# Kernel optimization log

Measured on AMD Instinct MI355X. Metric: run time of the kernel, lower is better.

Reference implementation:

```python
import jax, jax.numpy as jnp
import numpy as np

N_P, N_HE, N_E = 50000, 5000, 800000
D_IN, D_HID, D_OUT = 128, 256, 128
N_HEADS = 4
HEAD_DIM = D_HID // N_HEADS  # 64


def setup_inputs() -> dict:
    key = jax.random.key(0)
    ks = jax.random.split(key, 20)

    def xav(k, shape):
        fan_in, fan_out = shape[-2], shape[-1]
        lim = (6.0 / (fan_in + fan_out)) ** 0.5
        return jax.random.uniform(k, shape, jnp.float32, -lim, lim)

    return {
        "feat": jax.random.normal(ks[0], (N_P, D_IN), jnp.float32),
        "edge_w": jax.random.uniform(ks[1], (N_E,), jnp.float32),
        "Wself": xav(ks[2], (D_IN, D_OUT)), "bself": jnp.zeros((D_OUT,), jnp.float32),
        "Wclu": xav(ks[3], (D_IN, D_OUT)), "bclu": jnp.zeros((D_OUT,), jnp.float32),
        # 4 attention heads, each: Linear(D_IN->HEAD_DIM) -> ReLU -> Linear(HEAD_DIM->1) -> Sigmoid
        "Wh1": xav(ks[4], (N_HEADS, D_IN, HEAD_DIM)), "bh1": jnp.zeros((N_HEADS, HEAD_DIM), jnp.float32),
        "Wh2": xav(ks[5], (N_HEADS, HEAD_DIM, 1))[..., 0], "bh2": jnp.zeros((N_HEADS,), jnp.float32),
        "Wfuse": xav(ks[6], (N_HEADS, 1)),  # attn_fusion, no bias
        # fusion_attention MLP: 2*D_OUT -> D_HID -> D_HID//2 -> 2, softmax
        "Wf1": xav(ks[7], (2 * D_OUT, D_HID)), "bf1": jnp.zeros((D_HID,), jnp.float32),
        "Wf2": xav(ks[8], (D_HID, D_HID // 2)), "bf2": jnp.zeros((D_HID // 2,), jnp.float32),
        "Wf3": xav(ks[9], (D_HID // 2, 2)), "bf3": jnp.zeros((2,), jnp.float32),
        "edge_pid": jax.random.randint(ks[10], (N_E,), 0, N_P, jnp.int32),
        "edge_hid": jax.random.randint(ks[11], (N_E,), 0, N_HE, jnp.int32),
        "n_hyperedges": N_HE,
    }


def reference(feat, edge_w, Wself, bself, Wclu, bclu, Wh1, bh1, Wh2, bh2,
              Wfuse, Wf1, bf1, Wf2, bf2, Wf3, bf3,
              edge_pid, edge_hid, n_hyperedges):
    n_proteins = feat.shape[0]
    ew = edge_w[:, None]
    # Pass 1: protein -> hyperedge weighted gather-scatter (u_mul_e + sum)
    he_feat = jax.ops.segment_sum(feat[edge_pid] * ew, edge_hid, num_segments=n_hyperedges)  # [n_he, D_IN]
    # Multi-head MLP attention over hyperedge features
    h = jax.nn.relu(jnp.einsum('nd,hdk->hnk', he_feat, Wh1) + bh1[:, None, :])  # [H, n_he, hd]
    attn = jax.nn.sigmoid(jnp.einsum('hnk,hk->hn', h, Wh2) + bh2[:, None])      # [H, n_he]
    he_attn = attn.T @ Wfuse                                                    # [n_he, 1]
    he_weighted = he_feat * he_attn
    # Pass 2: hyperedge -> protein weighted gather-scatter
    cluster_feat = jax.ops.segment_sum(he_weighted[edge_hid] * ew, edge_pid, num_segments=n_proteins)  # [N, D_IN]
    # Transforms + fusion attention
    self_f = feat @ Wself + bself
    clu_f = cluster_feat @ Wclu + bclu
    cat = jnp.concatenate([self_f, clu_f], axis=-1)
    fw = jax.nn.softmax(
        jax.nn.relu(jax.nn.relu(cat @ Wf1 + bf1) @ Wf2 + bf2) @ Wf3 + bf3, axis=-1)  # [N, 2]
    fused = self_f * fw[:, 0:1] + clu_f * fw[:, 1:2]
    # residual: input_dim == output_dim so residual_proj is None (identity)
    return jax.nn.relu(fused + feat)
```

## Files before the change

### kernel.cpp

```cpp
#include <hip/hip_runtime.h>

#define N_P 50000
#define N_HE 5000
#define N_E 800000
#define D_IN 128
#define D_HID 256
#define N_HEADS 4
#define HEAD_DIM 64
#define CAP_HE 320
#define CAP_P  64
#define NTILE_TOT 3125
#define NCHUNK 782
#define CS2 264

typedef __attribute__((ext_vector_type(8))) short short8;
typedef __attribute__((ext_vector_type(8))) _Float16 half8;
typedef __attribute__((ext_vector_type(4))) float f32x4;

__device__ __forceinline__ short f2bs(float x) {
    union { float f; unsigned u; } v; v.f = x;
    unsigned r = (v.u + 0x7FFFu + ((v.u >> 16) & 1u)) >> 16;
    return (short)r;
}
__device__ __forceinline__ float bs2f(short s) {
    union { unsigned u; float f; } v; v.u = ((unsigned)(unsigned short)s) << 16;
    return v.f;
}
__device__ __forceinline__ short f2hs(float x) {
    union { _Float16 h; short s; } v; v.h = (_Float16)x; return v.s;
}

__global__ void k_zero_int(int* __restrict__ p, unsigned n) {
    unsigned i = blockIdx.x * blockDim.x + threadIdx.x;
    unsigned stride = gridDim.x * blockDim.x;
    for (; i < n; i += stride) p[i] = 0;
}

__global__ void k_prep(
    const float* __restrict__ Wself, const float* __restrict__ Wclu,
    const float* __restrict__ Wf1,   const float* __restrict__ Wf2,
    short* __restrict__ WselfT_hi, short* __restrict__ WselfT_lo,
    short* __restrict__ WcluT_hi,  short* __restrict__ WcluT_lo,
    short* __restrict__ Wf1T_h,
    short* __restrict__ Wf2T_h) {
    unsigned i = blockIdx.x * 256u + threadIdx.x;
    if (i < 16384u) {
        unsigned j = i >> 7, d = i & 127u;
        float v = Wself[d * 128 + j];
        short h = f2bs(v);
        WselfT_hi[i] = h; WselfT_lo[i] = f2bs(v - bs2f(h));
    } else if (i < 32768u) {
        unsigned ii = i - 16384u, j = ii >> 7, d = ii & 127u;
        float v = Wclu[d * 128 + j];
        short h = f2bs(v);
        WcluT_hi[ii] = h; WcluT_lo[ii] = f2bs(v - bs2f(h));
    } else if (i < 98304u) {
        unsigned ii = i - 32768u, j = ii >> 8, d = ii & 255u;
        Wf1T_h[ii] = f2hs(Wf1[d * 256 + j]);
    } else {
        unsigned ii = i - 98304u, j = ii >> 8, d = ii & 255u;
        Wf2T_h[ii] = f2hs(Wf2[d * 128 + j]);
    }
}

__global__ void k_bucket(
    const int* __restrict__ edge_pid, const int* __restrict__ edge_hid,
    const float* __restrict__ edge_w,
    int* __restrict__ cnt_he, int* __restrict__ cnt_p,
    int2* __restrict__ list_he, int2* __restrict__ list_p,
    int* __restrict__ ovf_he, int* __restrict__ ovf_he_cnt,
    int* __restrict__ ovf_p,  int* __restrict__ ovf_p_cnt) {
    unsigned e = blockIdx.x * blockDim.x + threadIdx.x;
    unsigned stride = gridDim.x * blockDim.x;
    for (; e < N_E; e += stride) {
        int h = edge_hid[e], p = edge_pid[e];
        int wbits = __float_as_int(edge_w[e]);
        int pos = atomicAdd(cnt_he + h, 1);
        if (pos < CAP_HE) list_he[h * CAP_HE + pos] = make_int2(p, wbits);
        else              ovf_he[atomicAdd(ovf_he_cnt, 1)] = (int)e;
        int pp = atomicAdd(cnt_p + p, 1);
        if (pp < CAP_P)   list_p[p * CAP_P + pp] = make_int2(h, wbits);
        else              ovf_p[atomicAdd(ovf_p_cnt, 1)] = (int)e;
    }
}

__global__ void k_he(
    const float* __restrict__ feat,
    const int* __restrict__ cnt_he, const int2* __restrict__ list_he,
    const int* __restrict__ ovf_he, const int* __restrict__ ovf_he_cnt,
    const float* __restrict__ edge_w,
    const int* __restrict__ edge_pid, const int* __restrict__ edge_hid,
    const float* __restrict__ Wh1, const float* __restrict__ bh1,
    const float* __restrict__ Wh2, const float* __restrict__ bh2,
    const float* __restrict__ Wfuse,
    float* __restrict__ he_weighted) {
    __shared__ float ptl[4][D_IN];
    __shared__ float hef[D_IN];
    __shared__ float attnv[N_HEADS];
    __shared__ float heattn;
    int h = blockIdx.x;
    int t = threadIdx.x;
    int wv = t >> 6, lane = t & 63;

    int n = cnt_he[h]; if (n > CAP_HE) n = CAP_HE;
    const int2* lst = list_he + (size_t)h * CAP_HE;
    float2 acc = make_float2(0.f, 0.f);
    #pragma unroll 4
    for (int k = wv; k < n; k += 4) {
        int2 pr = lst[k];
        float2 f = *(const float2*)(feat + (size_t)(unsigned)pr.x * D_IN + lane * 2);
        float w = __int_as_float(pr.y);
        acc.x += f.x * w; acc.y += f.y * w;
    }
    int oc = *ovf_he_cnt;
    for (int k = wv; k < oc; k += 4) {
        int e = ovf_he[k];
        if (edge_hid[e] == h) {
            float2 f = *(const float2*)(feat + (size_t)(unsigned)edge_pid[e] * D_IN + lane * 2);
            float w = edge_w[e];
            acc.x += f.x * w; acc.y += f.y * w;
        }
    }
    ptl[wv][lane * 2] = acc.x;
    ptl[wv][lane * 2 + 1] = acc.y;
    __syncthreads();
    if (t < D_IN) hef[t] = ptl[0][t] + ptl[1][t] + ptl[2][t] + ptl[3][t];
    __syncthreads();

    int head = wv, k = lane;
    float s = bh1[head * HEAD_DIM + k];
    for (int dd = 0; dd < D_IN; ++dd)
        s += hef[dd] * Wh1[(head * D_IN + dd) * HEAD_DIM + k];
    s = fmaxf(s, 0.f);
    float val = s * Wh2[head * HEAD_DIM + k];
    for (int off = 32; off; off >>= 1) val += __shfl_down(val, off);
    if (k == 0) {
        float x = val + bh2[head];
        attnv[head] = 1.f / (1.f + expf(-x));
    }
    __syncthreads();
    if (t == 0) {
        float ha = 0.f;
        #pragma unroll
        for (int hh = 0; hh < N_HEADS; ++hh) ha += attnv[hh] * Wfuse[hh];
        heattn = ha;
    }
    __syncthreads();
    if (t < D_IN) he_weighted[h * D_IN + t] = hef[t] * heattn;
}

__global__ void k_gather_clu(
    const float* __restrict__ he_weighted,
    const int* __restrict__ cnt_p, const int2* __restrict__ list_p,
    const int* __restrict__ ovf_p, const int* __restrict__ ovf_p_cnt,
    const float* __restrict__ edge_w,
    const int* __restrict__ edge_pid, const int* __restrict__ edge_hid,
    float* __restrict__ cluster_feat) {
    int p = blockIdx.x;
    int n = cnt_p[p]; if (n > CAP_P) n = CAP_P;
    const int2* lst = list_p + (size_t)p * CAP_P;
    int d = threadIdx.x;
    float acc = 0.f;
    #pragma unroll 4
    for (int k = 0; k < n; ++k) {
        int2 pr = lst[k];
        acc += he_weighted[(unsigned)pr.x * D_IN + d] * __int_as_float(pr.y);
    }
    int oc = *ovf_p_cnt;
    for (int k = 0; k < oc; ++k) {
        int e = ovf_p[k];
        if (edge_pid[e] == p)
            acc += he_weighted[(unsigned)edge_hid[e] * D_IN + d] * edge_w[e];
    }
    cluster_feat[p * D_IN + d] = acc;
}

__global__ __launch_bounds__(256, 2) void k_mlp1(
    const float* __restrict__ feat, const float* __restrict__ cluster_feat,
    const short* __restrict__ WselfT_hi, const short* __restrict__ WselfT_lo, const float* __restrict__ bself,
    const short* __restrict__ WcluT_hi,  const short* __restrict__ WcluT_lo,  const float* __restrict__ bclu,
    short* __restrict__ catF) {
    int t = threadIdx.x;
    int wv = t >> 6, lane = t & 63, col = lane & 15, q = lane >> 4;
    int m0 = blockIdx.x * 64;
    int tiles = NTILE_TOT - blockIdx.x * 4; if (tiles > 4) tiles = 4;
    const float* A = (wv < 2) ? feat : cluster_feat;
    const short* bHi = (wv < 2) ? WselfT_hi : WcluT_hi;
    const short* bLo = (wv < 2) ? WselfT_lo : WcluT_lo;
    const float* bias = (wv < 2) ? bself : bclu;
    int nb = (wv & 1) * 64;
    int cofs = (wv < 2) ? 0 : 128;

    for (int ih = 0; ih < 2; ++ih) {
        short8 Bh[2][4], Bl[2][4];
        float bv[2];
        #pragma unroll
        for (int i2 = 0; i2 < 2; ++i2) {
            int n = nb + (ih * 2 + i2) * 16 + col;
            bv[i2] = bias[n];
            #pragma unroll
            for (int ks = 0; ks < 4; ++ks) {
                int kb = ks * 32 + q * 8;
                Bh[i2][ks] = *(const short8*)&bHi[n * 128 + kb];
                Bl[i2][ks] = *(const short8*)&bLo[n * 128 + kb];
            }
        }
        for (int mt = 0; mt < tiles; ++mt) {
            int row = m0 + mt * 16 + col;
            f32x4 acc[2];
            acc[0] = (f32x4){0.f, 0.f, 0.f, 0.f};
            acc[1] = (f32x4){0.f, 0.f, 0.f, 0.f};
            #pragma unroll
            for (int ks = 0; ks < 4; ++ks) {
                int kb = ks * 32 + q * 8;
                const float* ap = A + (size_t)row * D_IN + kb;
                float4 a0 = *(const float4*)ap, a1 = *(const float4*)(ap + 4);
                float av[8] = {a0.x, a0.y, a0.z, a0.w, a1.x, a1.y, a1.z, a1.w};
                short8 ah, al;
                #pragma unroll
                for (int j = 0; j < 8; ++j) {
                    short h = f2bs(av[j]); ah[j] = h; al[j] = f2bs(av[j] - bs2f(h));
                }
                #pragma unroll
                for (int i2 = 0; i2 < 2; ++i2) {
                    acc[i2] = __builtin_amdgcn_mfma_f32_16x16x32_bf16(ah, Bh[i2][ks], acc[i2], 0, 0, 0);
                    acc[i2] = __builtin_amdgcn_mfma_f32_16x16x32_bf16(al, Bh[i2][ks], acc[i2], 0, 0, 0);
                    acc[i2] = __builtin_amdgcn_mfma_f32_16x16x32_bf16(ah, Bl[i2][ks], acc[i2], 0, 0, 0);
                }
            }
            #pragma unroll
            for (int i2 = 0; i2 < 2; ++i2) {
                int n = nb + (ih * 2 + i2) * 16 + col;
                #pragma unroll
                for (int r = 0; r < 4; ++r) {
                    float v = acc[i2][r] + bv[i2];
                    size_t o = (size_t)(m0 + mt * 16 + q * 4 + r) * 256 + cofs + n;
                    catF[o] = f2hs(v);
                }
            }
        }
    }
}

__global__ __launch_bounds__(256, 2) void k_mlp23(
    const short* __restrict__ catF,
    const short* __restrict__ Wf1T_h, const float* __restrict__ bf1,
    const short* __restrict__ Wf2T_h, const float* __restrict__ bf2,
    const float* __restrict__ Wf3, const float* __restrict__ bf3,
    const float* __restrict__ feat, float* __restrict__ out) {
    __shared__ __align__(16) short h1Hs[64 * CS2];
    __shared__ float fw[64 * 2];
    float* h2F = (float*)h1Hs;
    int t = threadIdx.x;
    int wv = t >> 6, lane = t & 63, col = lane & 15, q = lane >> 4;
    int m0 = blockIdx.x * 64;
    int tiles = NTILE_TOT - blockIdx.x * 4; if (tiles > 4) tiles = 4;
    int rows = tiles * 16;

    for (int ih = 0; ih < 2; ++ih) {
        half8 Bh[2][8];
        float bv[2];
        #pragma unroll
        for (int ii = 0; ii < 2; ++ii) {
            int n = wv * 64 + (ih * 2 + ii) * 16 + col;
            bv[ii] = bf1[n];
            #pragma unroll
            for (int ks = 0; ks < 8; ++ks) {
                int kb = ks * 32 + q * 8;
                Bh[ii][ks] = *(const half8*)&Wf1T_h[n * 256 + kb];
            }
        }
        for (int mt = 0; mt < tiles; ++mt) {
            int row = m0 + mt * 16 + col;
            f32x4 acc[2];
            acc[0] = (f32x4){0.f, 0.f, 0.f, 0.f};
            acc[1] = (f32x4){0.f, 0.f, 0.f, 0.f};
            #pragma unroll
            for (int ks = 0; ks < 8; ++ks) {
                int kb = ks * 32 + q * 8;
                half8 ah = *(const half8*)&catF[(size_t)row * 256 + kb];
                #pragma unroll
                for (int ii = 0; ii < 2; ++ii)
                    acc[ii] = __builtin_amdgcn_mfma_f32_16x16x32_f16(ah, Bh[ii][ks], acc[ii], 0, 0, 0);
            }
            #pragma unroll
            for (int ii = 0; ii < 2; ++ii) {
                int n = wv * 64 + (ih * 2 + ii) * 16 + col;
                #pragma unroll
                for (int r = 0; r < 4; ++r) {
                    float v = fmaxf(acc[ii][r] + bv[ii], 0.f);
                    int rl = mt * 16 + q * 4 + r;
                    h1Hs[rl * CS2 + n] = f2hs(v);
                }
            }
        }
    }
    __syncthreads();

    f32x4 acc2[2][4];
    #pragma unroll
    for (int ii = 0; ii < 2; ++ii)
        #pragma unroll
        for (int mt = 0; mt < 4; ++mt) acc2[ii][mt] = (f32x4){0.f, 0.f, 0.f, 0.f};
    for (int ii = 0; ii < 2; ++ii) {
        half8 Bh2[8];
        int n = wv * 32 + ii * 16 + col;
        #pragma unroll
        for (int ks = 0; ks < 8; ++ks) {
            int kb = ks * 32 + q * 8;
            Bh2[ks] = *(const half8*)&Wf2T_h[n * 256 + kb];
        }
        for (int mt = 0; mt < tiles; ++mt) {
            #pragma unroll
            for (int ks = 0; ks < 8; ++ks) {
                int kb = ks * 32 + q * 8;
                half8 ah = *(const half8*)&h1Hs[(mt * 16 + col) * CS2 + kb];
                acc2[ii][mt] = __builtin_amdgcn_mfma_f32_16x16x32_f16(ah, Bh2[ks], acc2[ii][mt], 0, 0, 0);
            }
        }
    }
    __syncthreads();

    #pragma unroll
    for (int ii = 0; ii < 2; ++ii) {
        int n = wv * 32 + ii * 16 + col;
        float bvv = bf2[n];
        for (int mt = 0; mt < tiles; ++mt) {
            #pragma unroll
            for (int r = 0; r < 4; ++r)
                h2F[(mt * 16 + q * 4 + r) * 132 + n] = fmaxf(acc2[ii][mt][r] + bvv, 0.f);
        }
    }
    __syncthreads();

    {
        int p = t >> 2, c = t & 3;
        if (p < rows) {
            float s0 = 0.f, s1 = 0.f;
            for (int n = c * 32; n < c * 32 + 32; ++n) {
                float h = h2F[p * 132 + n];
                s0 += h * Wf3[n * 2 + 0];
                s1 += h * Wf3[n * 2 + 1];
            }
            #pragma unroll
            for (int off = 2; off; off >>= 1) {
                s0 += __shfl_down(s0, off, 4);
                s1 += __shfl_down(s1, off, 4);
            }
            if (c == 0) {
                float l0 = s0 + bf3[0], l1 = s1 + bf3[1];
                float m = fmaxf(l0, l1);
                float e0 = expf(l0 - m), e1 = expf(l1 - m);
                float inv = 1.f / (e0 + e1);
                fw[p * 2 + 0] = e0 * inv;
                fw[p * 2 + 1] = e1 * inv;
            }
        }
    }
    __syncthreads();

    #pragma unroll
    for (int k = 0; k < 4; ++k) {
        int idx = t + k * 256;
        int rl = idx >> 4;
        int j = (idx & 15) * 8;
        if (rl < rows) {
            size_t ro = (size_t)(m0 + rl);
            half8 sf = *(const half8*)&catF[ro * 256 + j];
            half8 cf = *(const half8*)&catF[ro * 256 + 128 + j];
            const float* fp = feat + ro * D_IN + j;
            float4 f0 = *(const float4*)fp, f1 = *(const float4*)(fp + 4);
            float fe[8] = {f0.x, f0.y, f0.z, f0.w, f1.x, f1.y, f1.z, f1.w};
            float w0 = fw[rl * 2 + 0], w1 = fw[rl * 2 + 1];
            float o[8];
            #pragma unroll
            for (int qq = 0; qq < 8; ++qq) {
                float self_f = (float)sf[qq];
                float clu_f  = (float)cf[qq];
                o[qq] = fmaxf(self_f * w0 + clu_f * w1 + fe[qq], 0.f);
            }
            float* ob = out + ro * D_IN + j;
            *(float4*)ob = make_float4(o[0], o[1], o[2], o[3]);
            *(float4*)(ob + 4) = make_float4(o[4], o[5], o[6], o[7]);
        }
    }
}

extern "C" void kernel_launch(void* const* d_in, const int* in_sizes, int n_in,
                              void* d_out, int out_size, void* d_ws, size_t ws_size,
                              hipStream_t stream) {
    (void)in_sizes; (void)n_in; (void)out_size; (void)ws_size;
    const float* feat   = (const float*)d_in[0];
    const float* edge_w = (const float*)d_in[1];
    const float* Wself  = (const float*)d_in[2];
    const float* bself  = (const float*)d_in[3];
    const float* Wclu   = (const float*)d_in[4];
    const float* bclu   = (const float*)d_in[5];
    const float* Wh1    = (const float*)d_in[6];
    const float* bh1    = (const float*)d_in[7];
    const float* Wh2    = (const float*)d_in[8];
    const float* bh2    = (const float*)d_in[9];
    const float* Wfuse  = (const float*)d_in[10];
    const float* Wf1    = (const float*)d_in[11];
    const float* bf1_   = (const float*)d_in[12];
    const float* Wf2    = (const float*)d_in[13];
    const float* bf2_   = (const float*)d_in[14];
    const float* Wf3    = (const float*)d_in[15];
    const float* bf3_   = (const float*)d_in[16];
    const int* edge_pid = (const int*)d_in[17];
    const int* edge_hid = (const int*)d_in[18];
    float* out = (float*)d_out;

    float* he_feat      = (float*)d_ws;
    float* cluster_feat = he_feat + (size_t)N_HE * D_IN;
    int2* list_he = (int2*)(cluster_feat + (size_t)N_P * D_IN);
    int2* list_p  = list_he + (size_t)N_HE * CAP_HE;
    int* cnt_he  = (int*)(list_p + (size_t)N_P * CAP_P);
    int* cnt_p   = cnt_he + N_HE;
    int* ovf_he_cnt = cnt_p + N_P;
    int* ovf_p_cnt  = ovf_he_cnt + 1;
    int* ovf_he  = ovf_p_cnt + 1;
    int* ovf_p   = ovf_he + N_E;
    short* WselfT_hi = (short*)(ovf_p + N_E);
    short* WselfT_lo = WselfT_hi + 128 * 128;
    short* WcluT_hi  = WselfT_lo + 128 * 128;
    short* WcluT_lo  = WcluT_hi + 128 * 128;
    short* Wf1T_h    = WcluT_lo + 128 * 128;
    short* Wf2T_h    = Wf1T_h + 256 * 256;
    short* catF      = Wf2T_h + 128 * 256;

    k_prep<<<512, 256, 0, stream>>>(Wself, Wclu, Wf1, Wf2,
                                    WselfT_hi, WselfT_lo, WcluT_hi, WcluT_lo,
                                    Wf1T_h, Wf2T_h);
    k_zero_int<<<64, 256, 0, stream>>>(cnt_he, (unsigned)(N_HE + N_P + 2));
    k_bucket<<<2048, 256, 0, stream>>>(edge_pid, edge_hid, edge_w, cnt_he, cnt_p,
                                       list_he, list_p, ovf_he, ovf_he_cnt, ovf_p, ovf_p_cnt);
    k_he<<<N_HE, 256, 0, stream>>>(feat, cnt_he, list_he, ovf_he, ovf_he_cnt,
                                   edge_w, edge_pid, edge_hid,
                                   Wh1, bh1, Wh2, bh2, Wfuse, he_feat);
    k_gather_clu<<<N_P, 128, 0, stream>>>(he_feat, cnt_p, list_p, ovf_p, ovf_p_cnt,
                                          edge_w, edge_pid, edge_hid, cluster_feat);
    k_mlp1<<<NCHUNK, 256, 0, stream>>>(feat, cluster_feat,
                                       WselfT_hi, WselfT_lo, bself,
                                       WcluT_hi, WcluT_lo, bclu, catF);
    k_mlp23<<<NCHUNK, 256, 0, stream>>>(catF,
                                        Wf1T_h, bf1_,
                                        Wf2T_h, bf2_,
                                        Wf3, bf3_, feat, out);
}
```

Measured before the change: 427.3 us.

## Replace per-edge global-atomic bucketing with two-pass coarse binning

Edge bucketing into per-hyperedge and per-protein lists now first groups edges into coarse bins using shared-memory counting and block-level bin reservation, then a second pass scatters each bin into the final lists. Overflow records now carry packed (h,p,w) so the gather kernels no longer re-read edge arrays. This aims to cut random global atomic contention and improve write locality, at the cost of extra kernel launches, an extra read/write of edge records, and a bounded overflow buffer that could drop edges if capacities are exceeded.

```diff
diff --git a/kernel.cpp b/kernel.cpp
--- a/kernel.cpp
+++ b/kernel.cpp
@@ -12,6 +12,16 @@
 #define NTILE_TOT 3125
 #define NCHUNK 782
 #define CS2 264
+
+#define NBIN_HE 79
+#define HEB_SHIFT 6
+#define BINCAP_HE 16384
+#define NBIN_P 98
+#define PB_SHIFT 9
+#define BINCAP_P 12288
+#define BATCH 2048
+#define NBATCH 391
+#define OVF_CAP 8192
 
 typedef __attribute__((ext_vector_type(8))) short short8;
 typedef __attribute__((ext_vector_type(8))) _Float16 half8;
@@ -63,33 +73,100 @@
     }
 }
 
-__global__ void k_bucket(
+__global__ void k_binA(
     const int* __restrict__ edge_pid, const int* __restrict__ edge_hid,
     const float* __restrict__ edge_w,
-    int* __restrict__ cnt_he, int* __restrict__ cnt_p,
-    int2* __restrict__ list_he, int2* __restrict__ list_p,
-    int* __restrict__ ovf_he, int* __restrict__ ovf_he_cnt,
-    int* __restrict__ ovf_p,  int* __restrict__ ovf_p_cnt) {
-    unsigned e = blockIdx.x * blockDim.x + threadIdx.x;
-    unsigned stride = gridDim.x * blockDim.x;
-    for (; e < N_E; e += stride) {
-        int h = edge_hid[e], p = edge_pid[e];
-        int wbits = __float_as_int(edge_w[e]);
-        int pos = atomicAdd(cnt_he + h, 1);
-        if (pos < CAP_HE) list_he[h * CAP_HE + pos] = make_int2(p, wbits);
-        else              ovf_he[atomicAdd(ovf_he_cnt, 1)] = (int)e;
-        int pp = atomicAdd(cnt_p + p, 1);
-        if (pp < CAP_P)   list_p[p * CAP_P + pp] = make_int2(h, wbits);
-        else              ovf_p[atomicAdd(ovf_p_cnt, 1)] = (int)e;
+    int key_is_h, int shift, int nbin, int bincap,
+    int* __restrict__ bincnt, int2* __restrict__ bins,
+    int2* __restrict__ ovf, int* __restrict__ ovf_cnt) {
+    __shared__ int lcnt[128];
+    __shared__ int loffs[128];
+    __shared__ int gbase[128];
+    __shared__ int2 stage[BATCH];
+    __shared__ short tbin[BATCH];
+    int t = threadIdx.x;
+    unsigned base = (unsigned)blockIdx.x * BATCH;
+    int count = (int)min((unsigned)BATCH, N_E - base);
+    if (t < nbin) lcnt[t] = 0;
+    __syncthreads();
+
+    int b_[8], pos_[8]; int2 rec_[8]; bool v_[8];
+    #pragma unroll
+    for (int j = 0; j < 8; ++j) {
+        int i = j * 256 + t;
+        v_[j] = (i < count);
+        if (v_[j]) {
+            unsigned e = base + i;
+            int h = edge_hid[e], p = edge_pid[e];
+            int wbits = __float_as_int(edge_w[e]);
+            int b = (key_is_h ? h : p) >> shift;
+            b_[j] = b;
+            rec_[j] = make_int2(h | (p << 13), wbits);
+            pos_[j] = atomicAdd(&lcnt[b], 1);
+        }
+    }
+    __syncthreads();
+    if (t == 0) {
+        int s = 0;
+        for (int b = 0; b < nbin; ++b) { loffs[b] = s; s += lcnt[b]; }
+    }
+    if (t < nbin) gbase[t] = lcnt[t] ? atomicAdd(&bincnt[t], lcnt[t]) : 0;
+    __syncthreads();
+    #pragma unroll
+    for (int j = 0; j < 8; ++j) {
+        if (v_[j]) {
+            int idx = loffs[b_[j]] + pos_[j];
+            stage[idx] = rec_[j];
+            tbin[idx] = (short)b_[j];
+        }
+    }
+    __syncthreads();
+    for (int i = t; i < count; i += 256) {
+        int b = tbin[i];
+        int g = gbase[b] + (i - loffs[b]);
+        if (g < bincap) bins[(size_t)b * bincap + g] = stage[i];
+        else { int o = atomicAdd(ovf_cnt, 1); if (o < OVF_CAP) ovf[o] = stage[i]; }
+    }
+}
+
+__global__ void k_binB_he(
+    const int* __restrict__ bincnt, const int2* __restrict__ bins,
+    int* __restrict__ cnt_he, int2* __restrict__ list_he,
+    int2* __restrict__ ovf, int* __restrict__ ovf_cnt) {
+    int b = blockIdx.x;
+    int n = min(bincnt[b], BINCAP_HE);
+    const int2* src = bins + (size_t)b * BINCAP_HE;
+    for (int k = threadIdx.x; k < n; k += blockDim.x) {
+        int2 rec = src[k];
+        int h = rec.x & 8191;
+        int p = rec.x >> 13;
+        int pos = atomicAdd(&cnt_he[h], 1);
+        if (pos < CAP_HE) list_he[(size_t)h * CAP_HE + pos] = make_int2(p, rec.y);
+        else { int o = atomicAdd(ovf_cnt, 1); if (o < OVF_CAP) ovf[o] = rec; }
+    }
+}
+
+__global__ void k_binB_p(
+    const int* __restrict__ bincnt, const int2* __restrict__ bins,
+    int* __restrict__ cnt_p, int2* __restrict__ list_p,
+    int2* __restrict__ ovf, int* __restrict__ ovf_cnt) {
+    int b = blockIdx.x;
+    int n = min(bincnt[b], BINCAP_P);
+    const int2* src = bins + (size_t)b * BINCAP_P;
+    for (int k = threadIdx.x; k < n; k += blockDim.x) {
+        int2 rec = src[k];
+        int h = rec.x & 8191;
+        int p = rec.x >> 13;
+        int pos = atomicAdd(&cnt_p[p], 1);
+        if (pos < CAP_P) list_p[(size_t)p * CAP_P + pos] = make_int2(h, rec.y);
+        else { int o = atomicAdd(ovf_cnt, 1); if (o < OVF_CAP) ovf[o] = rec; }
     }
 }
 
 __global__ void k_he(
     const float* __restrict__ feat,
     const int* __restrict__ cnt_he, const int2* __restrict__ list_he,
-    const int* __restrict__ ovf_he, const int* __restrict__ ovf_he_cnt,
-    const float* __restrict__ edge_w,
-    const int* __restrict__ edge_pid, const int* __restrict__ edge_hid,
+    const int2* __restrict__ ovf_he, const int* __restrict__ ovf_he_cnt,
     const float* __restrict__ Wh1, const float* __restrict__ bh1,
     const float* __restrict__ Wh2, const float* __restrict__ bh2,
     const float* __restrict__ Wfuse,
@@ -112,12 +189,12 @@
         float w = __int_as_float(pr.y);
         acc.x += f.x * w; acc.y += f.y * w;
     }
-    int oc = *ovf_he_cnt;
+    int oc = min(*ovf_he_cnt, OVF_CAP);
     for (int k = wv; k < oc; k += 4) {
-        int e = ovf_he[k];
-        if (edge_hid[e] == h) {
-            float2 f = *(const float2*)(feat + (size_t)(unsigned)edge_pid[e] * D_IN + lane * 2);
-            float w = edge_w[e];
+        int2 rec = ovf_he[k];
+        if ((rec.x & 8191) == h) {
+            float2 f = *(const float2*)(feat + (size_t)(unsigned)(rec.x >> 13) * D_IN + lane * 2);
+            float w = __int_as_float(rec.y);
             acc.x += f.x * w; acc.y += f.y * w;
         }
     }
@@ -152,9 +229,7 @@
 __global__ void k_gather_clu(
     const float* __restrict__ he_weighted,
     const int* __restrict__ cnt_p, const int2* __restrict__ list_p,
-    const int* __restrict__ ovf_p, const int* __restrict__ ovf_p_cnt,
-    const float* __restrict__ edge_w,
-    const int* __restrict__ edge_pid, const int* __restrict__ edge_hid,
+    const int2* __restrict__ ovf_p, const int* __restrict__ ovf_p_cnt,
     float* __restrict__ cluster_feat) {
     int p = blockIdx.x;
     int n = cnt_p[p]; if (n > CAP_P) n = CAP_P;
@@ -166,11 +241,11 @@
         int2 pr = lst[k];
         acc += he_weighted[(unsigned)pr.x * D_IN + d] * __int_as_float(pr.y);
     }
-    int oc = *ovf_p_cnt;
+    int oc = min(*ovf_p_cnt, OVF_CAP);
     for (int k = 0; k < oc; ++k) {
-        int e = ovf_p[k];
-        if (edge_pid[e] == p)
-            acc += he_weighted[(unsigned)edge_hid[e] * D_IN + d] * edge_w[e];
+        int2 rec = ovf_p[k];
+        if ((rec.x >> 13) == p)
+            acc += he_weighted[(unsigned)(rec.x & 8191) * D_IN + d] * __int_as_float(rec.y);
     }
     cluster_feat[p * D_IN + d] = acc;
 }
@@ -415,13 +490,17 @@
     float* cluster_feat = he_feat + (size_t)N_HE * D_IN;
     int2* list_he = (int2*)(cluster_feat + (size_t)N_P * D_IN);
     int2* list_p  = list_he + (size_t)N_HE * CAP_HE;
-    int* cnt_he  = (int*)(list_p + (size_t)N_P * CAP_P);
-    int* cnt_p   = cnt_he + N_HE;
+    int2* binHE   = list_p + (size_t)N_P * CAP_P;
+    int2* binP    = binHE + (size_t)NBIN_HE * BINCAP_HE;
+    int2* ovf_he  = binP + (size_t)NBIN_P * BINCAP_P;
+    int2* ovf_p   = ovf_he + OVF_CAP;
+    int* cnt_he   = (int*)(ovf_p + OVF_CAP);
+    int* cnt_p    = cnt_he + N_HE;
     int* ovf_he_cnt = cnt_p + N_P;
     int* ovf_p_cnt  = ovf_he_cnt + 1;
-    int* ovf_he  = ovf_p_cnt + 1;
-    int* ovf_p   = ovf_he + N_E;
-    short* WselfT_hi = (short*)(ovf_p + N_E);
+    int* bincntHE = ovf_p_cnt + 1;
+    int* bincntP  = bincntHE + NBIN_HE;
+    short* WselfT_hi = (short*)(bincntP + NBIN_P);
     short* WselfT_lo = WselfT_hi + 128 * 128;
     short* WcluT_hi  = WselfT_lo + 128 * 128;
     short* WcluT_lo  = WcluT_hi + 128 * 128;
@@ -432,14 +511,22 @@
     k_prep<<<512, 256, 0, stream>>>(Wself, Wclu, Wf1, Wf2,
                                     WselfT_hi, WselfT_lo, WcluT_hi, WcluT_lo,
                                     Wf1T_h, Wf2T_h);
-    k_zero_int<<<64, 256, 0, stream>>>(cnt_he, (unsigned)(N_HE + N_P + 2));
-    k_bucket<<<2048, 256, 0, stream>>>(edge_pid, edge_hid, edge_w, cnt_he, cnt_p,
-                                       list_he, list_p, ovf_he, ovf_he_cnt, ovf_p, ovf_p_cnt);
+    k_zero_int<<<64, 256, 0, stream>>>(cnt_he,
+        (unsigned)(N_HE + N_P + 2 + NBIN_HE + NBIN_P));
+    k_binA<<<NBATCH, 256, 0, stream>>>(edge_pid, edge_hid, edge_w,
+                                       1, HEB_SHIFT, NBIN_HE, BINCAP_HE,
+                                       bincntHE, binHE, ovf_he, ovf_he_cnt);
+    k_binA<<<NBATCH, 256, 0, stream>>>(edge_pid, edge_hid, edge_w,
+                                       0, PB_SHIFT, NBIN_P, BINCAP_P,
+                                       bincntP, binP, ovf_p, ovf_p_cnt);
+    k_binB_he<<<NBIN_HE, 256, 0, stream>>>(bincntHE, binHE, cnt_he, list_he,
+                                           ovf_he, ovf_he_cnt);
+    k_binB_p<<<NBIN_P, 256, 0, stream>>>(bincntP, binP, cnt_p, list_p,
+                                         ovf_p, ovf_p_cnt);
     k_he<<<N_HE, 256, 0, stream>>>(feat, cnt_he, list_he, ovf_he, ovf_he_cnt,
-                                   edge_w, edge_pid, edge_hid,
                                    Wh1, bh1, Wh2, bh2, Wfuse, he_feat);
     k_gather_clu<<<N_P, 128, 0, stream>>>(he_feat, cnt_p, list_p, ovf_p, ovf_p_cnt,
-                                          edge_w, edge_pid, edge_hid, cluster_feat);
+                                          cluster_feat);
     k_mlp1<<<NCHUNK, 256, 0, stream>>>(feat, cluster_feat,
                                        WselfT_hi, WselfT_lo, bself,
                                        WcluT_hi, WcluT_lo, bclu, catF);
```

Result: no change. 433.1 us (+1.4%).
